# Kernel optimization log

Measured on AMD Instinct MI355X. Metric: run time of the kernel, lower is better.

Reference implementation:

```python
import jax, jax.numpy as jnp
import numpy as np

B, S, V = 32, 4096, 128
NSEG = S // 2 + 2  # rising-edge boundaries are at most ceil(S/2), so seg_id <= S//2


def sinusoidal_pe(seq_len, d_model, dtype=jnp.float32):
    pos = jnp.arange(seq_len, dtype=jnp.float32)[:, None]              # [S,1]
    div = jnp.exp(jnp.arange(0, d_model, 2, dtype=jnp.float32) * (-np.log(10000.0) / d_model))
    pe = jnp.zeros((seq_len, d_model), dtype=jnp.float32)
    pe = pe.at[:, 0::2].set(jnp.sin(pos * div))
    pe = pe.at[:, 1::2].set(jnp.cos(pos * div))
    return pe.astype(dtype)


def setup_inputs() -> dict:
    key = jax.random.key(0)
    ks = jax.random.split(key, 8)
    return {
        "bert_output": jax.random.normal(ks[0], (B, S, V), dtype=jnp.float32),
        "startpos": jax.random.uniform(ks[1], (B, S), dtype=jnp.float32),
        "Wq": jax.random.normal(ks[2], (V, V), dtype=jnp.float32) * 0.02,
        "bq": jax.random.normal(ks[3], (V,), dtype=jnp.float32) * 0.02,
        "Wk": jax.random.normal(ks[4], (V, V), dtype=jnp.float32) * 0.02,
        "bk": jax.random.normal(ks[5], (V,), dtype=jnp.float32) * 0.02,
        "Wv": jax.random.normal(ks[6], (V, V), dtype=jnp.float32) * 0.02,
        "bv": jax.random.normal(ks[7], (V,), dtype=jnp.float32) * 0.02,
    }


def reference(bert_output, startpos, Wq, bq, Wk, bk, Wv, bv):
    b, s, v = bert_output.shape
    pe = sinusoidal_pe(s, v, bert_output.dtype)
    # positionembedding2 then positionembedding1 (eval mode -> dropout is identity)
    x1 = bert_output + pe          # what gets concatenated at the end
    xseq = x1 + pe                 # per-row sequence fed to pooling and attention (pe added twice, as in source)

    # Rising-edge segment boundaries: mask[t] = start[t]>=0.5 and (t==0 or start[t-1]<0.5)
    ge = startpos >= 0.5
    prev = jnp.concatenate([jnp.zeros((b, 1), dtype=bool), ge[:, :-1]], axis=1)
    mask = ge & (~prev)                                     # [B,S]
    seg_id = jnp.cumsum(mask.astype(jnp.int32), axis=1)     # inclusive cumsum: token's segment index
    num_time_seq = jnp.sum(mask.astype(jnp.int32), axis=1) + 1

    # Mean-pool xseq per segment (segment_sum over flattened (batch, seg) ids)
    flat_ids = (jnp.arange(b, dtype=jnp.int32)[:, None] * NSEG + seg_id).reshape(-1)
    seg_sum = jax.ops.segment_sum(xseq.reshape(b * s, v), flat_ids, num_segments=b * NSEG)
    seg_cnt = jax.ops.segment_sum(jnp.ones((b * s,), xseq.dtype), flat_ids, num_segments=b * NSEG)
    seg_mean = (seg_sum / jnp.maximum(seg_cnt, 1.0)[:, None]).reshape(b, NSEG, v)

    # AttentionLayer (no softmax): out = (q @ K^T / sqrt(S)) @ V  ==  q @ (K^T V) / sqrt(S)
    q_seg = seg_mean @ Wq.T + bq                             # [B,NSEG,V]
    k = xseq @ Wk.T + bk                                     # [B,S,V]
    vv = xseq @ Wv.T + bv                                    # [B,S,V]
    kv = jnp.einsum("bsv,bsw->bvw", k, vv)                  # [B,V,V]
    q_tok = jnp.take_along_axis(q_seg, seg_id[..., None], axis=1)  # broadcast segment q to tokens [B,S,V]
    attn = jnp.einsum("btv,bvw->btw", q_tok, kv) / np.sqrt(float(s)).astype(np.float32)

    out = jnp.concatenate([attn, x1], axis=-1)               # [B,S,2V]
    return out, num_time_seq
```

## Files before the change

### kernel.cpp

```cpp
#include <hip/hip_runtime.h>
#include <hip/hip_bf16.h>

#define BB 32
#define SS 4096
#define VV 128
#define NSEG 2050
#define OUT_TAIL (BB*SS*2*VV)

#define PE_F      0u
#define SEGID_F   524288u
#define NSEGS_F   655360u
#define WQTA_F    655392u
#define WKA_F     671904u
#define ZT_F      688416u
#define ZB_F      966944u
#define C1OUT_F   971040u
#define C2OUT_F   1511712u
#define ATT_F     2036000u
#define GPART_F   ATT_F
#define SSUM_F    6234400u
#define SCNT_F    14631200u
#define SGLB_F    14696800u
#define GACC_F    14700896u

#define ATT_BYTE    ((size_t)ATT_F*4)
#define ZT_BYTE     ((size_t)ZT_F*4)
#define LDS_MAIN    132624

using bfrag8 = __attribute__((ext_vector_type(8))) short;
using usvec8 = __attribute__((ext_vector_type(8))) unsigned short;
using f32x4  = __attribute__((ext_vector_type(4))) float;

__device__ __forceinline__ unsigned short f2bf(float v){
  unsigned int u = __float_as_uint(v);
  u += 0x7fffu + ((u >> 16) & 1u);
  return (unsigned short)(u >> 16);
}
__device__ __forceinline__ float bf2f(unsigned short h){
  return __uint_as_float(((unsigned int)h) << 16);
}

__global__ void k_init(const float* __restrict__ Wq, const float* __restrict__ bq,
                       const float* __restrict__ Wk, const float* __restrict__ bk,
                       float* __restrict__ ws){
  int bx = blockIdx.x, tid = threadIdx.x;
  if (bx < 1024){
    int gid = bx*256 + tid;
    int t = gid >> 6, i = gid & 63;
    float dv = __expf(-0.14391156831212787f * (float)i);
    float ang = (float)t * dv;
    float s, c;
    __sincosf(ang, &s, &c);
    float2 o; o.x = s; o.y = c;
    ((float2*)(ws + PE_F))[(size_t)t*64 + i] = o;
  } else {
    int gid = (bx - 1024)*256 + tid;
    if (gid < 16384){
      int vv = gid >> 7, a = gid & 127;
      ws[WQTA_F + vv*128 + a] = Wq[a*128 + vv];
    } else if (gid < 16512){
      int a = gid - 16384;
      ws[WQTA_F + 128*128 + a] = bq[a];
    } else if (gid < 32896){
      int e = gid - 16512; int a = e >> 7, i = e & 127;
      ws[WKA_F + a*129 + i] = Wk[a*128 + i];
    } else if (gid < 33024){
      int a = gid - 32896;
      ws[WKA_F + a*129 + 128] = bk[a];
    }
  }
}

__global__ __launch_bounds__(1024) void k_scan(const float* __restrict__ sp,
                                               float* __restrict__ ws,
                                               float* __restrict__ out){
  int b = blockIdx.x, tid = threadIdx.x;
  __shared__ int wtot[16];
  const float* row = sp + (size_t)b*SS;
  float4 v4 = *(const float4*)(row + tid*4);
  float pv = (tid == 0) ? 0.f : row[tid*4 - 1];
  bool g0 = v4.x >= 0.5f, g1 = v4.y >= 0.5f, g2 = v4.z >= 0.5f, g3 = v4.w >= 0.5f;
  bool gp = (tid == 0) ? false : (pv >= 0.5f);
  int m0 = (g0 && !gp) ? 1 : 0;
  int m1 = (g1 && !g0) ? 1 : 0;
  int m2 = (g2 && !g1) ? 1 : 0;
  int m3 = (g3 && !g2) ? 1 : 0;
  int c0 = m0, c1 = c0+m1, c2 = c1+m2, c3 = c2+m3;
  int lane = tid & 63, wave = tid >> 6;
  int v = c3;
  #pragma unroll
  for (int off = 1; off < 64; off <<= 1){
    int u = __shfl_up(v, off);
    if (lane >= off) v += u;
  }
  if (lane == 63) wtot[wave] = v;
  __syncthreads();
  if (tid < 16){
    int x = wtot[tid];
    #pragma unroll
    for (int off = 1; off < 16; off <<= 1){
      int u = __shfl_up(x, off);
      if (tid >= off) x += u;
    }
    wtot[tid] = x;
  }
  __syncthreads();
  int woff = (wave == 0) ? 0 : wtot[wave-1];
  int excl = woff + v - c3;
  int4 o; o.x = excl+c0; o.y = excl+c1; o.z = excl+c2; o.w = excl+c3;
  *(int4*)((int*)ws + SEGID_F + (size_t)b*SS + tid*4) = o;
  if (tid == 1023){
    int total = woff + v;
    ((int*)ws)[NSEGS_F + b] = total + 1;
    out[OUT_TAIL + b] = (float)(total + 1);
  }
}

__global__ __launch_bounds__(1024) void k_main(const float* __restrict__ bert,
                                               float* __restrict__ ws,
                                               float* __restrict__ out){
  extern __shared__ char smem[];
  float* segacc = (float*)(smem + 65536);
  float* cntacc = (float*)(smem + 65536 + 66048);
  unsigned short* lseg = (unsigned short*)(smem + 65536 + 66048 + 516);

  const int tid = threadIdx.x;
  const int b = blockIdx.y, chunk = blockIdx.x;
  const int fgrp4 = tid & 31, trow = tid >> 5;

  const int* segid = (const int*)ws + SEGID_F + (size_t)b*SS;
  const float* pe = ws + PE_F;

  const int wave = tid >> 6, lane = tid & 63;
  const int mi = wave >> 1, njb = (wave & 1) * 4;
  const int l15 = lane & 15, l4 = lane >> 4;
  f32x4 acc[4];
  #pragma unroll
  for (int q = 0; q < 4; ++q) acc[q] = (f32x4){0.f,0.f,0.f,0.f};
  float sp_part = 0.f;
  const int sf = tid & 127, sgrp = tid >> 7;

  for (int sub = 0; sub < 2; ++sub){
    const int t0 = chunk*512 + sub*256;
    int seg0 = segid[t0];
    if (tid < 256) lseg[tid] = (unsigned short)(segid[t0 + tid] - seg0);
    int nl = segid[t0 + 255] - seg0 + 1;
    for (int idx = tid; idx < nl*32; idx += 1024) ((f32x4*)segacc)[idx] = (f32x4){0.f,0.f,0.f,0.f};
    if (tid < nl) cntacc[tid] = 0.f;
    __syncthreads();

    const int tb = t0 + trow*8;
    const float* bp = bert + ((size_t)(b*SS) + tb)*VV + fgrp4*4;
    const float* pp = pe + (size_t)tb*VV + fgrp4*4;
    float* op = out + ((size_t)(b*SS) + tb)*(2*VV) + VV + fgrp4*4;

    f32x4 racc = (f32x4){0.f,0.f,0.f,0.f};
    unsigned short xb[8][4];
    int cur = lseg[trow*8];
    float runlen = 0.f;
    #pragma unroll
    for (int i = 0; i < 8; ++i){
      int ls = lseg[trow*8 + i];
      if (ls != cur){
        #pragma unroll
        for (int j = 0; j < 4; ++j) unsafeAtomicAdd(&segacc[cur*128 + fgrp4*4 + j], racc[j]);
        if (fgrp4 == 0) unsafeAtomicAdd(&cntacc[cur], runlen);
        racc = (f32x4){0.f,0.f,0.f,0.f}; runlen = 0.f; cur = ls;
      }
      f32x4 bv = __builtin_nontemporal_load((const f32x4*)(bp + i*VV));
      f32x4 pv = *(const f32x4*)(pp + i*VV);
      f32x4 x1 = bv + pv;
      __builtin_nontemporal_store(x1, (f32x4*)(op + i*2*VV));
      f32x4 x = x1 + pv;
      racc += x;
      #pragma unroll
      for (int j = 0; j < 4; ++j) xb[i][j] = f2bf(x[j]);
      runlen += 1.f;
    }
    #pragma unroll
    for (int j = 0; j < 4; ++j) unsafeAtomicAdd(&segacc[cur*128 + fgrp4*4 + j], racc[j]);
    if (fgrp4 == 0) unsafeAtomicAdd(&cntacc[cur], runlen);

    #pragma unroll
    for (int j = 0; j < 4; ++j){
      int f = fgrp4*4 + j;
      int sw = (f ^ (f >> 2)) & 7;
      usvec8 v;
      #pragma unroll
      for (int i = 0; i < 8; ++i) v[i] = xb[i][j];
      *(usvec8*)(smem + f*512 + ((trow ^ sw) << 4)) = v;
    }
    __syncthreads();

    float* srow = ws + SSUM_F + ((size_t)(b*NSEG) + seg0)*128;
    for (int idx = tid; idx < nl*32; idx += 1024){
      int r = idx >> 5, c4 = idx & 31;
      f32x4 v = ((f32x4*)segacc)[idx];
      if (r == 0 || r == nl-1){
        #pragma unroll
        for (int j = 0; j < 4; ++j) unsafeAtomicAdd(&srow[r*128 + c4*4 + j], v[j]);
      } else {
        *(f32x4*)(srow + r*128 + c4*4) = v;
      }
    }
    if (tid < nl){
      float c = cntacc[tid];
      float* cp = ws + SCNT_F + (size_t)b*NSEG + seg0 + tid;
      if (tid == 0 || tid == nl-1) unsafeAtomicAdd(cp, c);
      else *cp = c;
    }
    for (int r = sgrp; r < nl; r += 8) sp_part += segacc[r*128 + sf];

    #pragma unroll
    for (int kk = 0; kk < 8; ++kk){
      int gr = kk*4 + l4;
      int fa = mi*16 + l15;
      bfrag8 aF = *(const bfrag8*)(smem + fa*512 + ((gr ^ ((fa ^ (fa>>2)) & 7)) << 4));
      #pragma unroll
      for (int q = 0; q < 4; ++q){
        int fb = (njb + q)*16 + l15;
        bfrag8 bF = *(const bfrag8*)(smem + fb*512 + ((gr ^ ((fb ^ (fb>>2)) & 7)) << 4));
        acc[q] = __builtin_amdgcn_mfma_f32_16x16x32_bf16(aF, bF, acc[q], 0, 0, 0);
      }
    }
    __syncthreads();
  }

  segacc[tid] = sp_part;
  __syncthreads();
  if (tid < 128){
    float s = 0.f;
    #pragma unroll
    for (int k = 0; k < 8; ++k) s += segacc[tid + 128*k];
    unsafeAtomicAdd(ws + SGLB_F + b*128 + tid, s);
  }

  float* gp = ws + GPART_F + ((size_t)(b*8 + chunk) << 14);
  #pragma unroll
  for (int q = 0; q < 4; ++q){
    #pragma unroll
    for (int r = 0; r < 4; ++r){
      int row = mi*16 + l4*4 + r;
      int col = (njb + q)*16 + l15;
      gp[row*128 + col] = acc[q][r];
    }
  }
}

__global__ __launch_bounds__(256) void k_greduce(float* __restrict__ ws){
  int b = blockIdx.y, idx = blockIdx.x*256 + threadIdx.x;
  const f32x4* gp = (const f32x4*)(ws + GPART_F + ((size_t)(b*8) << 14)) + idx;
  f32x4 a = (f32x4){0.f,0.f,0.f,0.f};
  #pragma unroll
  for (int c = 0; c < 8; ++c) a += gp[(size_t)c << 12];
  ((f32x4*)(ws + GACC_F + ((size_t)b << 14)))[idx] = a;
}

__global__ __launch_bounds__(256) void k_stage(int stage, float* __restrict__ ws,
                                               const float* __restrict__ Wv,
                                               const float* __restrict__ bv){
  __shared__ unsigned short Al[64*136];
  __shared__ unsigned short Bl[129*136];
  __shared__ float svals[128];
  __shared__ float bvv[64];
  int b = blockIdx.x, r0 = blockIdx.y*64, tid = threadIdx.x;
  const float* Asrc; int lda; int N, K;
  if (stage == 1){ N=129; K=128; Asrc = Wv; lda = 128; }
  else if (stage == 2){ N=128; K=129; Asrc = ws + C1OUT_F + (size_t)b*16896; lda = 132; }
  else { N=129; K=128; Asrc = ws + C2OUT_F + (size_t)b*16384; lda = 128; }

  const float* gacc = ws + GACC_F + (size_t)b*16384;
  const float* sg   = ws + SGLB_F + (size_t)b*128;
  for (int n = tid >> 1; n < N; n += 128){
    int ks = (tid & 1) * 65;
    int ke = min(K, ks + 65);
    const float* src;
    if (stage == 1) src = (n < 128) ? (gacc + (size_t)n*128) : sg;
    else if (stage == 2) src = ws + WKA_F + (size_t)n*129;
    else src = ws + WQTA_F + (size_t)n*128;
    for (int k = ks; k < ke; ++k) Bl[n*136 + k] = f2bf(src[k]);
  }
  {
    int m = tid >> 2;
    int ks = (tid & 3) * 34;
    int ke = min(K, ks + 34);
    for (int k = ks; k < ke; ++k) Al[m*136 + k] = f2bf(Asrc[(size_t)(r0+m)*lda + k]);
  }
  if (stage == 1){
    if (tid < 128) svals[tid] = sg[tid];
    if (tid >= 128 && tid < 192) bvv[tid-128] = bv[r0 + tid - 128];
  }
  __syncthreads();

  int wave = tid >> 6, lane = tid & 63, l15 = lane & 15, l4 = lane >> 4;
  f32x4 acc[9];
  #pragma unroll
  for (int j = 0; j < 9; ++j) acc[j] = (f32x4){0.f,0.f,0.f,0.f};
  #pragma unroll
  for (int kk = 0; kk < 4; ++kk){
    int k = kk*32 + l4*8;
    bfrag8 aF = *(const bfrag8*)&Al[(wave*16 + l15)*136 + k];
    #pragma unroll
    for (int j = 0; j < 9; ++j){
      bfrag8 bF = *(const bfrag8*)&Bl[(j*16 + l15)*136 + k];
      acc[j] = __builtin_amdgcn_mfma_f32_16x16x32_bf16(aF, bF, acc[j], 0, 0, 0);
    }
  }
  unsigned short* zt = (unsigned short*)((char*)ws + ZT_BYTE);
  #pragma unroll
  for (int j = 0; j < 9; ++j){
    #pragma unroll
    for (int r = 0; r < 4; ++r){
      int lrow = wave*16 + l4*4 + r;
      int m = r0 + lrow;
      int n = j*16 + l15;
      float v = acc[j][r];
      if (K > 128) v += bf2f(Al[lrow*136 + 128]) * bf2f(Bl[n*136 + 128]);
      if (stage == 1){
        if (n < 129){
          float sx = (n < 128) ? svals[n] : 4096.0f;
          ws[C1OUT_F + (size_t)b*16896 + m*132 + n] = v + bvv[lrow]*sx;
        }
      } else if (stage == 2){
        if (n < 128) ws[C2OUT_F + (size_t)b*16384 + m*128 + n] = v;
      } else {
        float z = v * 0.015625f;
        if (n < 128) zt[(size_t)b*17408 + m*136 + n] = f2bf(z);
        else if (n == 128) ws[ZB_F + (size_t)b*128 + m] = z;
      }
    }
  }
}

__global__ __launch_bounds__(256) void k_attn(float* __restrict__ ws){
  int b = blockIdx.y, g0 = blockIdx.x * 64, tid = threadIdx.x;
  int nseg = ((const int*)ws)[NSEGS_F + b];
  if (g0 >= nseg) return;
  __shared__ unsigned short Albs[64*136];
  __shared__ unsigned short Blbs[128*136];
  __shared__ float zbs[128];
  {
    int row = tid >> 2, part = tid & 3;
    int g = g0 + row;
    float rc = 1.f;
    const float* ssum = ws + SSUM_F + ((size_t)(b*NSEG + g))*128;
    if (g < NSEG){ float c = ws[SCNT_F + (size_t)b*NSEG + g]; rc = 1.f / fmaxf(c, 1.f); }
    #pragma unroll
    for (int j = 0; j < 8; ++j){
      int cix = part*32 + j*4;
      float4 v;
      if (g < NSEG) v = *(const float4*)(ssum + cix);
      else { v.x=0.f; v.y=0.f; v.z=0.f; v.w=0.f; }
      unsigned short* dst = &Albs[row*136 + cix];
      dst[0] = f2bf(v.x*rc); dst[1] = f2bf(v.y*rc); dst[2] = f2bf(v.z*rc); dst[3] = f2bf(v.w*rc);
    }
  }
  {
    const unsigned int* src = (const unsigned int*)((const char*)ws + ZT_BYTE + (size_t)b*34816);
    unsigned int* dst = (unsigned int*)Blbs;
    for (int i = tid; i < 8704; i += 256) dst[i] = src[i];
  }
  if (tid < 128) zbs[tid] = ws[ZB_F + (size_t)b*128 + tid];
  __syncthreads();
  int wave = tid >> 6, lane = tid & 63, l15 = lane & 15, l4 = lane >> 4;
  f32x4 acc[8];
  #pragma unroll
  for (int q = 0; q < 8; ++q) acc[q] = (f32x4){0.f,0.f,0.f,0.f};
  #pragma unroll
  for (int kk = 0; kk < 4; ++kk){
    int k = kk*32 + l4*8;
    bfrag8 aF = *(const bfrag8*)&Albs[(wave*16 + l15)*136 + k];
    #pragma unroll
    for (int q = 0; q < 8; ++q){
      bfrag8 bF = *(const bfrag8*)&Blbs[(q*16 + l15)*136 + k];
      acc[q] = __builtin_amdgcn_mfma_f32_16x16x32_bf16(aF, bF, acc[q], 0, 0, 0);
    }
  }
  unsigned short* att = (unsigned short*)((char*)ws + ATT_BYTE);
  #pragma unroll
  for (int q = 0; q < 8; ++q){
    int w = q*16 + l15;
    float zb = zbs[w];
    #pragma unroll
    for (int r = 0; r < 4; ++r){
      int g = g0 + wave*16 + l4*4 + r;
      if (g < NSEG) att[((size_t)(b*NSEG) + g)*128 + w] = f2bf(acc[q][r] + zb);
    }
  }
}

__global__ __launch_bounds__(256) void k_out(const float* __restrict__ ws,
                                             float* __restrict__ out){
  int b = blockIdx.y, c0 = blockIdx.x * 512, tid = threadIdx.x;
  __shared__ unsigned short lsg[512];
  const int* segid = (const int*)ws + SEGID_F + (size_t)b*SS;
  lsg[tid] = (unsigned short)segid[c0 + tid];
  lsg[tid + 256] = (unsigned short)segid[c0 + tid + 256];
  __syncthreads();
  int fgrp = tid & 31, trow = tid >> 5;
  const unsigned short* att = (const unsigned short*)((const char*)ws + ATT_BYTE);
  #pragma unroll 4
  for (int i = 0; i < 64; ++i){
    int tl = i*8 + trow;
    int g = lsg[tl];
    const unsigned short* ap = att + ((size_t)(b*NSEG) + g)*128 + fgrp*4;
    uint2 raw = *(const uint2*)ap;
    f32x4 o;
    o[0] = bf2f((unsigned short)(raw.x & 0xffffu));
    o[1] = bf2f((unsigned short)(raw.x >> 16));
    o[2] = bf2f((unsigned short)(raw.y & 0xffffu));
    o[3] = bf2f((unsigned short)(raw.y >> 16));
    __builtin_nontemporal_store(o, (f32x4*)(out + ((size_t)(b*SS) + c0 + tl)*(2*VV) + fgrp*4));
  }
}

extern "C" void kernel_launch(void* const* d_in, const int* in_sizes, int n_in,
                              void* d_out, int out_size, void* d_ws, size_t ws_size,
                              hipStream_t stream) {
  const float* bert     = (const float*)d_in[0];
  const float* startpos = (const float*)d_in[1];
  const float* Wq       = (const float*)d_in[2];
  const float* bq       = (const float*)d_in[3];
  const float* Wk       = (const float*)d_in[4];
  const float* bk       = (const float*)d_in[5];
  const float* Wv       = (const float*)d_in[6];
  const float* bv       = (const float*)d_in[7];
  float* out = (float*)d_out;
  float* ws  = (float*)d_ws;

  (void)hipFuncSetAttribute(reinterpret_cast<const void*>(k_main),
                            hipFuncAttributeMaxDynamicSharedMemorySize, LDS_MAIN);

  k_init<<<1153, 256, 0, stream>>>(Wq, bq, Wk, bk, ws);
  k_scan<<<32, 1024, 0, stream>>>(startpos, ws, out);
  k_main<<<dim3(8, 32), 1024, LDS_MAIN, stream>>>(bert, ws, out);
  k_greduce<<<dim3(16, 32), 256, 0, stream>>>(ws);
  k_stage<<<dim3(32, 2), 256, 0, stream>>>(1, ws, Wv, bv);
  k_stage<<<dim3(32, 2), 256, 0, stream>>>(2, ws, Wv, bv);
  k_stage<<<dim3(32, 2), 256, 0, stream>>>(3, ws, Wv, bv);
  k_attn<<<dim3(33, 32), 256, 0, stream>>>(ws);
  k_out<<<dim3(8, 32), 256, 0, stream>>>(ws, out);
}
```

Baseline: 284.5 us.

## Fuse scan into init and merge greduce plus three stage GEMMs into one kernel

The segment-boundary scan now runs inside the init kernel as extra 1024-thread blocks. The partial-Gram reduction and the three chained small GEMM stages are collapsed into a single kernel that keeps each intermediate in LDS as bf16 instead of writing it to workspace and relaunching. This removes five launches and the global round-trips of the intermediates. In exchange, the per-block (b, row-half) fused kernel redundantly reduces the full 128x128 Gram partials for both row halves, keeps only 64 blocks running, and rounds the intermediates to bf16 in LDS.

After: 266.6 us. 6.3% less time.

```diff
diff --git a/kernel.cpp b/kernel.cpp
--- a/kernel.cpp
+++ b/kernel.cpp
@@ -14,14 +14,11 @@
 #define WKA_F     671904u
 #define ZT_F      688416u
 #define ZB_F      966944u
-#define C1OUT_F   971040u
-#define C2OUT_F   1511712u
 #define ATT_F     2036000u
 #define GPART_F   ATT_F
 #define SSUM_F    6234400u
 #define SCNT_F    14631200u
 #define SGLB_F    14696800u
-#define GACC_F    14700896u
 
 #define ATT_BYTE    ((size_t)ATT_F*4)
 #define ZT_BYTE     ((size_t)ZT_F*4)
@@ -40,12 +37,56 @@
   return __uint_as_float(((unsigned int)h) << 16);
 }
 
-__global__ void k_init(const float* __restrict__ Wq, const float* __restrict__ bq,
-                       const float* __restrict__ Wk, const float* __restrict__ bk,
-                       float* __restrict__ ws){
+__global__ __launch_bounds__(1024) void k_init(const float* __restrict__ Wq, const float* __restrict__ bq,
+                                               const float* __restrict__ Wk, const float* __restrict__ bk,
+                                               const float* __restrict__ sp,
+                                               float* __restrict__ ws, float* __restrict__ out){
   int bx = blockIdx.x, tid = threadIdx.x;
-  if (bx < 1024){
-    int gid = bx*256 + tid;
+  if (bx < 32){
+    int b = bx;
+    __shared__ int wtot[16];
+    const float* row = sp + (size_t)b*SS;
+    float4 v4 = *(const float4*)(row + tid*4);
+    float pv = (tid == 0) ? 0.f : row[tid*4 - 1];
+    bool g0 = v4.x >= 0.5f, g1 = v4.y >= 0.5f, g2 = v4.z >= 0.5f, g3 = v4.w >= 0.5f;
+    bool gp = (tid == 0) ? false : (pv >= 0.5f);
+    int m0 = (g0 && !gp) ? 1 : 0;
+    int m1 = (g1 && !g0) ? 1 : 0;
+    int m2 = (g2 && !g1) ? 1 : 0;
+    int m3 = (g3 && !g2) ? 1 : 0;
+    int c0 = m0, c1 = c0+m1, c2 = c1+m2, c3 = c2+m3;
+    int lane = tid & 63, wave = tid >> 6;
+    int v = c3;
+    #pragma unroll
+    for (int off = 1; off < 64; off <<= 1){
+      int u = __shfl_up(v, off);
+      if (lane >= off) v += u;
+    }
+    if (lane == 63) wtot[wave] = v;
+    __syncthreads();
+    if (tid < 16){
+      int x = wtot[tid];
+      #pragma unroll
+      for (int off = 1; off < 16; off <<= 1){
+        int u = __shfl_up(x, off);
+        if (tid >= off) x += u;
+      }
+      wtot[tid] = x;
+    }
+    __syncthreads();
+    int woff = (wave == 0) ? 0 : wtot[wave-1];
+    int excl = woff + v - c3;
+    int4 o; o.x = excl+c0; o.y = excl+c1; o.z = excl+c2; o.w = excl+c3;
+    *(int4*)((int*)ws + SEGID_F + (size_t)b*SS + tid*4) = o;
+    if (tid == 1023){
+      int total = woff + v;
+      ((int*)ws)[NSEGS_F + b] = total + 1;
+      out[OUT_TAIL + b] = (float)(total + 1);
+    }
+    return;
+  }
+  if (bx < 288){
+    int gid = (bx - 32)*1024 + tid;
     int t = gid >> 6, i = gid & 63;
     float dv = __expf(-0.14391156831212787f * (float)i);
     float ang = (float)t * dv;
@@ -54,7 +95,7 @@
     float2 o; o.x = s; o.y = c;
     ((float2*)(ws + PE_F))[(size_t)t*64 + i] = o;
   } else {
-    int gid = (bx - 1024)*256 + tid;
+    int gid = (bx - 288)*1024 + tid;
     if (gid < 16384){
       int vv = gid >> 7, a = gid & 127;
       ws[WQTA_F + vv*128 + a] = Wq[a*128 + vv];
@@ -68,51 +109,6 @@
       int a = gid - 32896;
       ws[WKA_F + a*129 + 128] = bk[a];
     }
-  }
-}
-
-__global__ __launch_bounds__(1024) void k_scan(const float* __restrict__ sp,
-                                               float* __restrict__ ws,
-                                               float* __restrict__ out){
-  int b = blockIdx.x, tid = threadIdx.x;
-  __shared__ int wtot[16];
-  const float* row = sp + (size_t)b*SS;
-  float4 v4 = *(const float4*)(row + tid*4);
-  float pv = (tid == 0) ? 0.f : row[tid*4 - 1];
-  bool g0 = v4.x >= 0.5f, g1 = v4.y >= 0.5f, g2 = v4.z >= 0.5f, g3 = v4.w >= 0.5f;
-  bool gp = (tid == 0) ? false : (pv >= 0.5f);
-  int m0 = (g0 && !gp) ? 1 : 0;
-  int m1 = (g1 && !g0) ? 1 : 0;
-  int m2 = (g2 && !g1) ? 1 : 0;
-  int m3 = (g3 && !g2) ? 1 : 0;
-  int c0 = m0, c1 = c0+m1, c2 = c1+m2, c3 = c2+m3;
-  int lane = tid & 63, wave = tid >> 6;
-  int v = c3;
-  #pragma unroll
-  for (int off = 1; off < 64; off <<= 1){
-    int u = __shfl_up(v, off);
-    if (lane >= off) v += u;
-  }
-  if (lane == 63) wtot[wave] = v;
-  __syncthreads();
-  if (tid < 16){
-    int x = wtot[tid];
-    #pragma unroll
-    for (int off = 1; off < 16; off <<= 1){
-      int u = __shfl_up(x, off);
-      if (tid >= off) x += u;
-    }
-    wtot[tid] = x;
-  }
-  __syncthreads();
-  int woff = (wave == 0) ? 0 : wtot[wave-1];
-  int excl = woff + v - c3;
-  int4 o; o.x = excl+c0; o.y = excl+c1; o.z = excl+c2; o.w = excl+c3;
-  *(int4*)((int*)ws + SEGID_F + (size_t)b*SS + tid*4) = o;
-  if (tid == 1023){
-    int total = woff + v;
-    ((int*)ws)[NSEGS_F + b] = total + 1;
-    out[OUT_TAIL + b] = (float)(total + 1);
   }
 }
 
@@ -247,16 +243,7 @@
   }
 }
 
-__global__ __launch_bounds__(256) void k_greduce(float* __restrict__ ws){
-  int b = blockIdx.y, idx = blockIdx.x*256 + threadIdx.x;
-  const f32x4* gp = (const f32x4*)(ws + GPART_F + ((size_t)(b*8) << 14)) + idx;
-  f32x4 a = (f32x4){0.f,0.f,0.f,0.f};
-  #pragma unroll
-  for (int c = 0; c < 8; ++c) a += gp[(size_t)c << 12];
-  ((f32x4*)(ws + GACC_F + ((size_t)b << 14)))[idx] = a;
-}
-
-__global__ __launch_bounds__(256) void k_stage(int stage, float* __restrict__ ws,
+__global__ __launch_bounds__(256) void k_fused(float* __restrict__ ws,
                                                const float* __restrict__ Wv,
                                                const float* __restrict__ bv){
   __shared__ unsigned short Al[64*136];
@@ -264,36 +251,33 @@
   __shared__ float svals[128];
   __shared__ float bvv[64];
   int b = blockIdx.x, r0 = blockIdx.y*64, tid = threadIdx.x;
-  const float* Asrc; int lda; int N, K;
-  if (stage == 1){ N=129; K=128; Asrc = Wv; lda = 128; }
-  else if (stage == 2){ N=128; K=129; Asrc = ws + C1OUT_F + (size_t)b*16896; lda = 132; }
-  else { N=129; K=128; Asrc = ws + C2OUT_F + (size_t)b*16384; lda = 128; }
-
-  const float* gacc = ws + GACC_F + (size_t)b*16384;
-  const float* sg   = ws + SGLB_F + (size_t)b*128;
-  for (int n = tid >> 1; n < N; n += 128){
-    int ks = (tid & 1) * 65;
-    int ke = min(K, ks + 65);
-    const float* src;
-    if (stage == 1) src = (n < 128) ? (gacc + (size_t)n*128) : sg;
-    else if (stage == 2) src = ws + WKA_F + (size_t)n*129;
-    else src = ws + WQTA_F + (size_t)n*128;
-    for (int k = ks; k < ke; ++k) Bl[n*136 + k] = f2bf(src[k]);
+  const float* sg = ws + SGLB_F + (size_t)b*128;
+  int wave = tid >> 6, lane = tid & 63, l15 = lane & 15, l4 = lane >> 4;
+
+  {
+    const f32x4* gq = (const f32x4*)(ws + GPART_F + ((size_t)(b*8) << 14));
+    for (int e = tid; e < 4096; e += 256){
+      f32x4 a = (f32x4){0.f,0.f,0.f,0.f};
+      #pragma unroll
+      for (int c = 0; c < 8; ++c) a += gq[((size_t)c << 12) + e];
+      int row = e >> 5, c4 = e & 31;
+      unsigned short* dst = &Bl[row*136 + c4*4];
+      dst[0]=f2bf(a[0]); dst[1]=f2bf(a[1]); dst[2]=f2bf(a[2]); dst[3]=f2bf(a[3]);
+    }
+    if (tid < 128) Bl[128*136 + tid] = f2bf(sg[tid]);
   }
   {
     int m = tid >> 2;
     int ks = (tid & 3) * 34;
-    int ke = min(K, ks + 34);
-    for (int k = ks; k < ke; ++k) Al[m*136 + k] = f2bf(Asrc[(size_t)(r0+m)*lda + k]);
-  }
-  if (stage == 1){
-    if (tid < 128) svals[tid] = sg[tid];
-    if (tid >= 128 && tid < 192) bvv[tid-128] = bv[r0 + tid - 128];
-  }
-  __syncthreads();
-
-  int wave = tid >> 6, lane = tid & 63, l15 = lane & 15, l4 = lane >> 4;
+    int ke = min(128, ks + 34);
+    for (int k = ks; k < ke; ++k) Al[m*136 + k] = f2bf(Wv[(size_t)(r0+m)*128 + k]);
+  }
+  if (tid < 128) svals[tid] = sg[tid];
+  if (tid >= 128 && tid < 192) bvv[tid-128] = bv[r0 + tid - 128];
+  __syncthreads();
+
   f32x4 acc[9];
+
   #pragma unroll
   for (int j = 0; j < 9; ++j) acc[j] = (f32x4){0.f,0.f,0.f,0.f};
   #pragma unroll
@@ -306,6 +290,81 @@
       acc[j] = __builtin_amdgcn_mfma_f32_16x16x32_bf16(aF, bF, acc[j], 0, 0, 0);
     }
   }
+  #pragma unroll
+  for (int j = 0; j < 9; ++j){
+    #pragma unroll
+    for (int r = 0; r < 4; ++r){
+      int lrow = wave*16 + l4*4 + r;
+      int n = j*16 + l15;
+      if (n < 129){
+        float sx = (n < 128) ? svals[n] : 4096.0f;
+        Al[lrow*136 + n] = f2bf(acc[j][r] + bvv[lrow]*sx);
+      }
+    }
+  }
+  __syncthreads();
+
+  for (int n = tid >> 1; n < 128; n += 128){
+    int ks = (tid & 1) * 65;
+    int ke = min(129, ks + 65);
+    const float* src = ws + WKA_F + (size_t)n*129;
+    for (int k = ks; k < ke; ++k) Bl[n*136 + k] = f2bf(src[k]);
+  }
+  __syncthreads();
+
+  #pragma unroll
+  for (int j = 0; j < 9; ++j) acc[j] = (f32x4){0.f,0.f,0.f,0.f};
+  #pragma unroll
+  for (int kk = 0; kk < 4; ++kk){
+    int k = kk*32 + l4*8;
+    bfrag8 aF = *(const bfrag8*)&Al[(wave*16 + l15)*136 + k];
+    #pragma unroll
+    for (int j = 0; j < 8; ++j){
+      bfrag8 bF = *(const bfrag8*)&Bl[(j*16 + l15)*136 + k];
+      acc[j] = __builtin_amdgcn_mfma_f32_16x16x32_bf16(aF, bF, acc[j], 0, 0, 0);
+    }
+  }
+  #pragma unroll
+  for (int j = 0; j < 8; ++j){
+    #pragma unroll
+    for (int r = 0; r < 4; ++r){
+      int lrow = wave*16 + l4*4 + r;
+      int n = j*16 + l15;
+      float v = acc[j][r] + bf2f(Al[lrow*136 + 128]) * bf2f(Bl[n*136 + 128]);
+      acc[j][r] = v;
+    }
+  }
+  #pragma unroll
+  for (int j = 0; j < 8; ++j){
+    #pragma unroll
+    for (int r = 0; r < 4; ++r){
+      int lrow = wave*16 + l4*4 + r;
+      int n = j*16 + l15;
+      if (n < 128) Al[lrow*136 + n] = f2bf(acc[j][r]);
+    }
+  }
+  __syncthreads();
+
+  for (int n = tid >> 1; n < 129; n += 128){
+    int ks = (tid & 1) * 65;
+    int ke = min(128, ks + 65);
+    const float* src = ws + WQTA_F + (size_t)n*128;
+    for (int k = ks; k < ke; ++k) Bl[n*136 + k] = f2bf(src[k]);
+  }
+  __syncthreads();
+
+  #pragma unroll
+  for (int j = 0; j < 9; ++j) acc[j] = (f32x4){0.f,0.f,0.f,0.f};
+  #pragma unroll
+  for (int kk = 0; kk < 4; ++kk){
+    int k = kk*32 + l4*8;
+    bfrag8 aF = *(const bfrag8*)&Al[(wave*16 + l15)*136 + k];
+    #pragma unroll
+    for (int j = 0; j < 9; ++j){
+      bfrag8 bF = *(const bfrag8*)&Bl[(j*16 + l15)*136 + k];
+      acc[j] = __builtin_amdgcn_mfma_f32_16x16x32_bf16(aF, bF, acc[j], 0, 0, 0);
+    }
+  }
   unsigned short* zt = (unsigned short*)((char*)ws + ZT_BYTE);
   #pragma unroll
   for (int j = 0; j < 9; ++j){
@@ -314,20 +373,9 @@
       int lrow = wave*16 + l4*4 + r;
       int m = r0 + lrow;
       int n = j*16 + l15;
-      float v = acc[j][r];
-      if (K > 128) v += bf2f(Al[lrow*136 + 128]) * bf2f(Bl[n*136 + 128]);
-      if (stage == 1){
-        if (n < 129){
-          float sx = (n < 128) ? svals[n] : 4096.0f;
-          ws[C1OUT_F + (size_t)b*16896 + m*132 + n] = v + bvv[lrow]*sx;
-        }
-      } else if (stage == 2){
-        if (n < 128) ws[C2OUT_F + (size_t)b*16384 + m*128 + n] = v;
-      } else {
-        float z = v * 0.015625f;
-        if (n < 128) zt[(size_t)b*17408 + m*136 + n] = f2bf(z);
-        else if (n == 128) ws[ZB_F + (size_t)b*128 + m] = z;
-      }
+      float z = acc[j][r] * 0.015625f;
+      if (n < 128) zt[(size_t)b*17408 + m*136 + n] = f2bf(z);
+      else if (n == 128) ws[ZB_F + (size_t)b*128 + m] = z;
     }
   }
 }
@@ -431,13 +479,9 @@
   (void)hipFuncSetAttribute(reinterpret_cast<const void*>(k_main),
                             hipFuncAttributeMaxDynamicSharedMemorySize, LDS_MAIN);
 
-  k_init<<<1153, 256, 0, stream>>>(Wq, bq, Wk, bk, ws);
-  k_scan<<<32, 1024, 0, stream>>>(startpos, ws, out);
+  k_init<<<321, 1024, 0, stream>>>(Wq, bq, Wk, bk, startpos, ws, out);
   k_main<<<dim3(8, 32), 1024, LDS_MAIN, stream>>>(bert, ws, out);
-  k_greduce<<<dim3(16, 32), 256, 0, stream>>>(ws);
-  k_stage<<<dim3(32, 2), 256, 0, stream>>>(1, ws, Wv, bv);
-  k_stage<<<dim3(32, 2), 256, 0, stream>>>(2, ws, Wv, bv);
-  k_stage<<<dim3(32, 2), 256, 0, stream>>>(3, ws, Wv, bv);
+  k_fused<<<dim3(32, 2), 256, 0, stream>>>(ws, Wv, bv);
   k_attn<<<dim3(33, 32), 256, 0, stream>>>(ws);
   k_out<<<dim3(8, 32), 256, 0, stream>>>(ws, out);
 }
```
